# Kernel optimization log

Hardware: AMD Instinct MI355X
Metric: run time of the kernel (lower is better)

## Reference

```python
import jax, jax.numpy as jnp
import numpy as np

B, L, D = 16, 1024, 768

def setup_inputs() -> dict:
    key = jax.random.key(0)
    ks = jax.random.split(key, 6)
    s = 1.0 / np.sqrt(D)  # torch Linear default init scale
    return {
        "h": jax.random.normal(ks[0], (B, L, D), dtype=jnp.float32),
        "q": jax.random.normal(ks[1], (B, L, D), dtype=jnp.float32),
        "w1_w": jax.random.uniform(ks[2], (L, D), jnp.float32, -s, s),
        "w1_b": jax.random.uniform(ks[3], (L,), jnp.float32, -s, s),
        "w2_w": jax.random.uniform(ks[4], (L, D), jnp.float32, -s, s),
        "w2_b": jax.random.uniform(ks[5], (L,), jnp.float32, -s, s),
    }

def reference(h, q, w1_w, w1_b, w2_w, w2_b):
    # w1h: [B, L, l], w2q: [B, L, l] -> permuted [B, l, L]
    w1h = jnp.einsum('bsd,ld->bsl', h, w1_w) + w1_b
    w2q = jnp.einsum('btd,ld->btl', q, w2_w) + w2_b
    w3hq = jnp.einsum('bsd,btd->bst', h, q)           # [B, L, L]
    a = w1h + jnp.swapaxes(w2q, 1, 2) + w3hq          # [B, L, L]
    p = jax.nn.softmax(a, axis=2)
    c = jnp.einsum('bst,btd->bsd', p, q)              # [B, L, D]
    m = jnp.max(a, axis=2)                            # [B, L]
    p2 = jax.nn.softmax(m, axis=1)                    # [B, L]
    qc = h * p2[:, :, None]                           # [B, L, D]
    return jnp.concatenate([h, c, h * c, qc * c], axis=2)  # [B, L, 4D]
```

## Files before the change

### kernel.cpp

```cpp
#include <hip/hip_runtime.h>
#include <stdint.h>

#define B_  16
#define L_  1024
#define D_  768
#define K1_ 1536

typedef unsigned short u16;
typedef __attribute__((ext_vector_type(4))) float f32x4;
typedef __attribute__((ext_vector_type(8))) _Float16 f16x8;

__device__ __forceinline__ u16 f2h(float x){
    return __builtin_bit_cast(u16, (_Float16)x);
}

__device__ __forceinline__ void gload_lds16(const void* g, void* l){
    __builtin_amdgcn_global_load_lds((const __attribute__((address_space(1))) void*)g,
                                     (__attribute__((address_space(3))) void*)l, 16, 0, 0);
}

__global__ __launch_bounds__(256) void prep(const float* __restrict__ h, const float* __restrict__ q,
    const float* __restrict__ w1w, const float* __restrict__ w2w,
    u16* __restrict__ hH, u16* __restrict__ wH, u16* __restrict__ qH,
    u16* __restrict__ w1h, u16* __restrict__ qT, int b0, int nb)
{
    __shared__ float tile[32][33];
    int bb = blockIdx.z, bg = b0 + bb;
    int t0 = blockIdx.x * 32, d0 = blockIdx.y * 32;
    int tid = threadIdx.x;
    int r  = tid >> 3;
    int c4 = (tid & 7) * 4;
    int t = t0 + r, d = d0 + c4;
    size_t goff = (size_t)t * D_ + d;

    float4 qv  = *(const float4*)(q   + (size_t)bg * L_ * D_ + goff);
    float4 hv  = *(const float4*)(h   + (size_t)bg * L_ * D_ + goff);
    float4 w2v = *(const float4*)(w2w + goff);

    tile[r][c4 + 0] = qv.x; tile[r][c4 + 1] = qv.y;
    tile[r][c4 + 2] = qv.z; tile[r][c4 + 3] = qv.w;

    size_t o = ((size_t)bb * L_ + t) * D_ + d;
    ushort4 a;
    a.x = f2h(hv.x); a.y = f2h(hv.y); a.z = f2h(hv.z); a.w = f2h(hv.w);
    *(ushort4*)(hH + o) = a;
    a.x = f2h(hv.x + w2v.x); a.y = f2h(hv.y + w2v.y);
    a.z = f2h(hv.z + w2v.z); a.w = f2h(hv.w + w2v.w);
    *(ushort4*)(wH + o) = a;
    a.x = f2h(qv.x); a.y = f2h(qv.y); a.z = f2h(qv.z); a.w = f2h(qv.w);
    *(ushort4*)(qH + o) = a;
    if (bb == 0){
        float4 w1v = *(const float4*)(w1w + goff);
        a.x = f2h(w1v.x); a.y = f2h(w1v.y); a.z = f2h(w1v.z); a.w = f2h(w1v.w);
        *(ushort4*)(w1h + goff) = a;
    }
    __syncthreads();
    int dr = tid >> 3;
    int tc = (tid & 7) * 4;
    ushort4 b;
    b.x = f2h(tile[tc + 0][dr]); b.y = f2h(tile[tc + 1][dr]);
    b.z = f2h(tile[tc + 2][dr]); b.w = f2h(tile[tc + 3][dr]);
    *(ushort4*)(qT + (size_t)bb * D_ * L_ + (size_t)(d0 + dr) * L_ + t0 + tc) = b;
}

__global__ __launch_bounds__(256) void gemm1(
    const u16* __restrict__ hH, const u16* __restrict__ wH,
    const u16* __restrict__ qH, const u16* __restrict__ w1h,
    const float* __restrict__ w1b, const float* __restrict__ w2b,
    u16* __restrict__ pT, float* __restrict__ mT, float* __restrict__ sT)
{
    __shared__ u16 ldsA[128 * 64];
    __shared__ u16 ldsB[128 * 64];
    int nwg = gridDim.x;
    int o = blockIdx.x;
    int wg = (o & 7) * (nwg >> 3) + (o >> 3);
    int bb = wg >> 6;
    int tl = wg & 63;
    int sm = tl >> 3, tn = tl & 7;
    int s0 = sm * 128, t0 = tn * 128;
    int tid = threadIdx.x;
    int lane = tid & 63, wid = tid >> 6;
    int wm = wid >> 1, wn = wid & 1;
    int l15 = lane & 15, l4 = lane >> 4;

    const u16* hHb = hH + (size_t)bb * L_ * D_;
    const u16* wHb = wH + (size_t)bb * L_ * D_;
    const u16* qHb = qH + (size_t)bb * L_ * D_;

    f32x4 acc[4][4];
    #pragma unroll
    for (int m = 0; m < 4; m++)
        #pragma unroll
        for (int n = 0; n < 4; n++)
            acc[m][n] = (f32x4){0.f, 0.f, 0.f, 0.f};

    for (int kb = 0; kb < K1_; kb += 64){
        bool inH = (kb < D_);
        const u16* Asrc = inH ? hHb : wHb;
        const u16* Bsrc = inH ? w1h : qHb;
        int koff = inH ? kb : (kb - D_);
        #pragma unroll
        for (int j = 0; j < 4; j++){
            int n = j * 256 + tid;
            int row = n >> 3, c = n & 7;
            int cc = c ^ (row & 7);
            int k = koff + cc * 8;
            gload_lds16(Asrc + (size_t)(s0 + row) * D_ + k, &ldsA[(j * 256 + wid * 64) * 8]);
            gload_lds16(Bsrc + (size_t)(t0 + row) * D_ + k, &ldsB[(j * 256 + wid * 64) * 8]);
        }
        __syncthreads();
        #pragma unroll
        for (int kk = 0; kk < 2; kk++){
            f16x8 af[4], bf[4];
            #pragma unroll
            for (int m = 0; m < 4; m++){
                int row = wm * 64 + m * 16 + l15;
                int c = kk * 4 + l4;
                af[m] = *(const f16x8*)&ldsA[(row * 8 + (c ^ (row & 7))) * 8];
            }
            #pragma unroll
            for (int n = 0; n < 4; n++){
                int row = wn * 64 + n * 16 + l15;
                int c = kk * 4 + l4;
                bf[n] = *(const f16x8*)&ldsB[(row * 8 + (c ^ (row & 7))) * 8];
            }
            #pragma unroll
            for (int m = 0; m < 4; m++)
                #pragma unroll
                for (int n = 0; n < 4; n++)
                    acc[m][n] = __builtin_amdgcn_mfma_f32_16x16x32_f16(af[m], bf[n], acc[m][n], 0, 0, 0);
        }
        __syncthreads();
    }

    u16* pRow = pT + (size_t)bb * L_ * L_;
    #pragma unroll
    for (int m = 0; m < 4; m++){
        #pragma unroll
        for (int r = 0; r < 4; r++){
            int s = s0 + wm * 64 + m * 16 + l4 * 4 + r;
            float w2v = w2b[s];
            float v[4];
            float tmax = -1e30f;
            #pragma unroll
            for (int n = 0; n < 4; n++){
                int tcol = t0 + wn * 64 + n * 16 + l15;
                v[n] = acc[m][n][r] + w1b[tcol] + w2v;
                tmax = fmaxf(tmax, v[n]);
            }
            #pragma unroll
            for (int o2 = 1; o2 < 16; o2 <<= 1)
                tmax = fmaxf(tmax, __shfl_xor(tmax, o2));
            float e[4];
            float gsum = 0.f;
            #pragma unroll
            for (int n = 0; n < 4; n++){
                e[n] = __expf(v[n] - tmax);
                gsum += e[n];
            }
            #pragma unroll
            for (int n = 0; n < 4; n++){
                int tcol = t0 + wn * 64 + n * 16 + l15;
                pRow[(size_t)s * L_ + tcol] = f2h(e[n]);
            }
            #pragma unroll
            for (int o2 = 1; o2 < 16; o2 <<= 1)
                gsum += __shfl_xor(gsum, o2);
            if (l15 == 0){
                size_t mo = ((size_t)bb * L_ + s) * 16 + tn * 2 + wn;
                mT[mo] = tmax;
                sT[mo] = gsum;
            }
        }
    }
}

__global__ __launch_bounds__(1024) void p2k(const float* __restrict__ mT, const float* __restrict__ sT,
                                            float* __restrict__ p2, float* __restrict__ sc, int b0)
{
    __shared__ float red[16];
    int bb = blockIdx.x, bg = b0 + bb;
    int tid = threadIdx.x;
    const float4* mv = (const float4*)(mT + ((size_t)bb * L_ + tid) * 16);
    float4 m0 = mv[0], m1 = mv[1], m2 = mv[2], m3 = mv[3];
    float mj[16] = {m0.x, m0.y, m0.z, m0.w, m1.x, m1.y, m1.z, m1.w,
                    m2.x, m2.y, m2.z, m2.w, m3.x, m3.y, m3.z, m3.w};
    float v = mj[0];
    #pragma unroll
    for (int i = 1; i < 16; i++) v = fmaxf(v, mj[i]);

    float mx = v;
    #pragma unroll
    for (int o = 32; o; o >>= 1) mx = fmaxf(mx, __shfl_xor(mx, o));
    if ((tid & 63) == 0) red[tid >> 6] = mx;
    __syncthreads();
    float m2g = red[0];
    #pragma unroll
    for (int i = 1; i < 16; i++) m2g = fmaxf(m2g, red[i]);
    float e = __expf(v - m2g);
    float sum = e;
    #pragma unroll
    for (int o = 32; o; o >>= 1) sum += __shfl_xor(sum, o);
    __syncthreads();
    if ((tid & 63) == 0) red[tid >> 6] = sum;
    __syncthreads();
    float st = 0.f;
    #pragma unroll
    for (int i = 0; i < 16; i++) st += red[i];
    p2[(size_t)bg * L_ + tid] = e / st;

    const float4* sv = (const float4*)(sT + ((size_t)bb * L_ + tid) * 16);
    float4 s0v = sv[0], s1v = sv[1], s2v = sv[2], s3v = sv[3];
    float sj[16] = {s0v.x, s0v.y, s0v.z, s0v.w, s1v.x, s1v.y, s1v.z, s1v.w,
                    s2v.x, s2v.y, s2v.z, s2v.w, s3v.x, s3v.y, s3v.z, s3v.w};
    float ej[16];
    float S = 0.f;
    #pragma unroll
    for (int j = 0; j < 16; j++){
        ej[j] = __expf(mj[j] - v);
        S += sj[j] * ej[j];
    }
    float invS = 1.0f / S;
    float* scb = sc + (size_t)bb * 16 * L_;
    #pragma unroll
    for (int j = 0; j < 16; j++)
        scb[j * L_ + tid] = ej[j] * invS;
}

__global__ __launch_bounds__(256) void gemm2(const u16* __restrict__ pT, const u16* __restrict__ qT,
    const float* __restrict__ sc, float* __restrict__ out, int b0)
{
    __shared__ u16 ldsA[128 * 64];
    __shared__ u16 ldsB[128 * 64];
    int nwg = gridDim.x;
    int o = blockIdx.x;
    int wg = (o & 7) * (nwg >> 3) + (o >> 3);
    int bb = wg / 48;
    int tl = wg % 48;
    int sm = tl / 6, dn = tl % 6;
    int s0 = sm * 128, d0 = dn * 128;
    int tid = threadIdx.x;
    int lane = tid & 63, wid = tid >> 6;
    int wm = wid >> 1, wn = wid & 1;
    int l15 = lane & 15, l4 = lane >> 4;

    const u16* Ab = pT + (size_t)bb * L_ * L_;
    const u16* Bb = qT + (size_t)bb * D_ * L_;
    const float* scb = sc + (size_t)bb * 16 * L_;

    f32x4 acc[4][4];
    #pragma unroll
    for (int m = 0; m < 4; m++)
        #pragma unroll
        for (int n = 0; n < 4; n++)
            acc[m][n] = (f32x4){0.f, 0.f, 0.f, 0.f};

    for (int kb = 0; kb < L_; kb += 64){
        int jg = kb >> 6;
        #pragma unroll
        for (int j = 0; j < 4; j++){
            int n = j * 256 + tid;
            int row = n >> 3, c = n & 7;
            int cc = c ^ (row & 7);
            gload_lds16(Ab + (size_t)(s0 + row) * L_ + kb + cc * 8, &ldsA[(j * 256 + wid * 64) * 8]);
        }
        #pragma unroll
        for (int j = 0; j < 4; j++){
            int n = j * 256 + tid;
            int row = n >> 3, c = n & 7;
            int cc = c ^ (row & 7);
            gload_lds16(Bb + (size_t)(d0 + row) * L_ + kb + cc * 8, &ldsB[(j * 256 + wid * 64) * 8]);
        }
        _Float16 sch[4];
        #pragma unroll
        for (int m = 0; m < 4; m++)
            sch[m] = (_Float16)scb[(size_t)jg * L_ + s0 + wm * 64 + m * 16 + l15];
        __syncthreads();
        #pragma unroll
        for (int kk = 0; kk < 2; kk++){
            f16x8 af[4], bf[4];
            #pragma unroll
            for (int m = 0; m < 4; m++){
                int row = wm * 64 + m * 16 + l15;
                int c = kk * 4 + l4;
                af[m] = *(const f16x8*)&ldsA[(row * 8 + (c ^ (row & 7))) * 8];
                af[m] = af[m] * sch[m];
            }
            #pragma unroll
            for (int n = 0; n < 4; n++){
                int row = wn * 64 + n * 16 + l15;
                int c = kk * 4 + l4;
                bf[n] = *(const f16x8*)&ldsB[(row * 8 + (c ^ (row & 7))) * 8];
            }
            #pragma unroll
            for (int m = 0; m < 4; m++)
                #pragma unroll
                for (int n = 0; n < 4; n++)
                    acc[m][n] = __builtin_amdgcn_mfma_f32_16x16x32_f16(af[m], bf[n], acc[m][n], 0, 0, 0);
        }
        __syncthreads();
    }

    float* oC = out + ((size_t)(b0 + bb) * L_) * (4 * D_) + D_;
    #pragma unroll
    for (int m = 0; m < 4; m++){
        int sbase = s0 + wm * 64 + m * 16 + l4 * 4;
        #pragma unroll
        for (int r = 0; r < 4; r++){
            int s = sbase + r;
            #pragma unroll
            for (int n = 0; n < 4; n++){
                int d = d0 + wn * 64 + n * 16 + l15;
                oC[(size_t)s * (4 * D_) + d] = acc[m][n][r];
            }
        }
    }
}

__global__ __launch_bounds__(192) void epi(const float* __restrict__ h,
    const float* __restrict__ p2, float* __restrict__ out, int b0)
{
    int rowid = blockIdx.x;
    int bb = rowid >> 10, s = rowid & 1023;
    int bg = b0 + bb;
    float p2v = p2[(size_t)bg * L_ + s];
    const float* hR = h + ((size_t)bg * L_ + s) * D_;
    float* oR = out + ((size_t)bg * L_ + s) * (4 * D_);
    int d = threadIdx.x * 4;
    float4 cv = *(const float4*)(oR + D_ + d);
    float4 hv = *(const float4*)(hR + d);
    float4 hc = {hv.x * cv.x, hv.y * cv.y, hv.z * cv.z, hv.w * cv.w};
    float4 qc = {p2v * hc.x, p2v * hc.y, p2v * hc.z, p2v * hc.w};
    *(float4*)(oR + d)          = hv;
    *(float4*)(oR + 2 * D_ + d) = hc;
    *(float4*)(oR + 3 * D_ + d) = qc;
}

extern "C" void kernel_launch(void* const* d_in, const int* in_sizes, int n_in,
                              void* d_out, int out_size, void* d_ws, size_t ws_size,
                              hipStream_t stream)
{
    const float* h   = (const float*)d_in[0];
    const float* q   = (const float*)d_in[1];
    const float* w1w = (const float*)d_in[2];
    const float* w1b = (const float*)d_in[3];
    const float* w2w = (const float*)d_in[4];
    const float* w2b = (const float*)d_in[5];
    float* out = (float*)d_out;

    const size_t szPlane = (size_t)L_ * D_ * 2;
    const size_t szM     = (size_t)B_ * L_ * 4;
    const size_t perB_pT = (size_t)L_ * L_ * 2;
    const size_t perB_s  = (size_t)L_ * 16 * 4;
    const size_t perB = 4 * szPlane + perB_pT + 3 * perB_s;
    const size_t fixed = szPlane + szM;

    int NB = 1;
    if (ws_size > fixed){
        size_t nbc = (ws_size - fixed) / perB;
        NB = (nbc >= 16) ? 16 : (nbc < 1 ? 1 : (int)nbc);
    }

    char* p = (char*)d_ws;
    u16*   w1h  = (u16*)p;   p += szPlane;
    float* p2   = (float*)p; p += szM;
    float* mT   = (float*)p; p += perB_s * NB;
    float* sT   = (float*)p; p += perB_s * NB;
    float* sc   = (float*)p; p += perB_s * NB;
    u16*   hH   = (u16*)p;   p += szPlane * NB;
    u16*   wH   = (u16*)p;   p += szPlane * NB;
    u16*   qH   = (u16*)p;   p += szPlane * NB;
    u16*   qT   = (u16*)p;   p += szPlane * NB;
    u16*   pT   = (u16*)p;

    for (int b0 = 0; b0 < B_; b0 += NB){
        int nb = (B_ - b0 < NB) ? (B_ - b0) : NB;
        prep  <<<dim3(32, 24, nb), 256, 0, stream>>>(h, q, w1w, w2w, hH, wH, qH, w1h, qT, b0, nb);
        gemm1 <<<dim3(64 * nb), 256, 0, stream>>>(hH, wH, qH, w1h, w1b, w2b, pT, mT, sT);
        p2k   <<<dim3(nb), 1024, 0, stream>>>(mT, sT, p2, sc, b0);
        gemm2 <<<dim3(48 * nb), 256, 0, stream>>>(pT, qT, sc, out, b0);
        epi   <<<dim3(nb * 1024), 192, 0, stream>>>(h, p2, out, b0);
    }
}
```

Before: 217.6 us.

## Enlarge gemm1 tiles to 256x256 with double-buffered LDS prefetch

```diff
diff --git a/kernel.cpp b/kernel.cpp
--- a/kernel.cpp
+++ b/kernel.cpp
@@ -63,88 +63,106 @@
     *(ushort4*)(qT + (size_t)bb * D_ * L_ + (size_t)(d0 + dr) * L_ + t0 + tc) = b;
 }
 
-__global__ __launch_bounds__(256) void gemm1(
+__global__ __launch_bounds__(512) void gemm1(
     const u16* __restrict__ hH, const u16* __restrict__ wH,
     const u16* __restrict__ qH, const u16* __restrict__ w1h,
     const float* __restrict__ w1b, const float* __restrict__ w2b,
     u16* __restrict__ pT, float* __restrict__ mT, float* __restrict__ sT)
 {
-    __shared__ u16 ldsA[128 * 64];
-    __shared__ u16 ldsB[128 * 64];
+    __shared__ u16 ldsA[2][256 * 64];
+    __shared__ u16 ldsB[2][256 * 64];
     int nwg = gridDim.x;
     int o = blockIdx.x;
     int wg = (o & 7) * (nwg >> 3) + (o >> 3);
-    int bb = wg >> 6;
-    int tl = wg & 63;
-    int sm = tl >> 3, tn = tl & 7;
-    int s0 = sm * 128, t0 = tn * 128;
+    int bb = wg >> 4;
+    int tl = wg & 15;
+    int smb = tl >> 2, tnb = tl & 3;
+    int s0 = smb * 256, t0 = tnb * 256;
     int tid = threadIdx.x;
     int lane = tid & 63, wid = tid >> 6;
-    int wm = wid >> 1, wn = wid & 1;
+    int wm2 = wid >> 2, wn2 = wid & 3;
     int l15 = lane & 15, l4 = lane >> 4;
 
     const u16* hHb = hH + (size_t)bb * L_ * D_;
     const u16* wHb = wH + (size_t)bb * L_ * D_;
     const u16* qHb = qH + (size_t)bb * L_ * D_;
 
-    f32x4 acc[4][4];
-    #pragma unroll
-    for (int m = 0; m < 4; m++)
+    f32x4 acc[8][4];
+    #pragma unroll
+    for (int m = 0; m < 8; m++)
         #pragma unroll
         for (int n = 0; n < 4; n++)
             acc[m][n] = (f32x4){0.f, 0.f, 0.f, 0.f};
 
-    for (int kb = 0; kb < K1_; kb += 64){
+    auto stage = [&](int t){
+        int kb = t * 64;
         bool inH = (kb < D_);
-        const u16* Asrc = inH ? hHb : wHb;
-        const u16* Bsrc = inH ? w1h : qHb;
+        const u16* As = inH ? hHb : wHb;
+        const u16* Bs = inH ? w1h : qHb;
         int koff = inH ? kb : (kb - D_);
-        #pragma unroll
-        for (int j = 0; j < 4; j++){
-            int n = j * 256 + tid;
-            int row = n >> 3, c = n & 7;
+        int buf = t & 1;
+        #pragma unroll
+        for (int q = 0; q < 4; q++){
+            int idx = q * 512 + tid;
+            int row = idx >> 3, c = idx & 7;
             int cc = c ^ (row & 7);
-            int k = koff + cc * 8;
-            gload_lds16(Asrc + (size_t)(s0 + row) * D_ + k, &ldsA[(j * 256 + wid * 64) * 8]);
-            gload_lds16(Bsrc + (size_t)(t0 + row) * D_ + k, &ldsB[(j * 256 + wid * 64) * 8]);
-        }
-        __syncthreads();
+            int dst = (q * 512 + wid * 64) * 8;
+            gload_lds16(As + (size_t)(s0 + row) * D_ + koff + cc * 8, &ldsA[buf][dst]);
+            gload_lds16(Bs + (size_t)(t0 + row) * D_ + koff + cc * 8, &ldsB[buf][dst]);
+        }
+    };
+
+    stage(0);
+    asm volatile("s_waitcnt vmcnt(0)" ::: "memory");
+    __builtin_amdgcn_s_barrier();
+
+    for (int t = 0; t < 24; t++){
+        if (t + 1 < 24) stage(t + 1);
+        int bsel = t & 1;
         #pragma unroll
         for (int kk = 0; kk < 2; kk++){
-            f16x8 af[4], bf[4];
-            #pragma unroll
-            for (int m = 0; m < 4; m++){
-                int row = wm * 64 + m * 16 + l15;
+            f16x8 bf[4];
+            #pragma unroll
+            for (int n = 0; n < 4; n++){
+                int row = wn2 * 64 + n * 16 + l15;
                 int c = kk * 4 + l4;
-                af[m] = *(const f16x8*)&ldsA[(row * 8 + (c ^ (row & 7))) * 8];
-            }
-            #pragma unroll
-            for (int n = 0; n < 4; n++){
-                int row = wn * 64 + n * 16 + l15;
-                int c = kk * 4 + l4;
-                bf[n] = *(const f16x8*)&ldsB[(row * 8 + (c ^ (row & 7))) * 8];
-            }
-            #pragma unroll
-            for (int m = 0; m < 4; m++)
+                bf[n] = *(const f16x8*)&ldsB[bsel][(row * 8 + (c ^ (row & 7))) * 8];
+            }
+            #pragma unroll
+            for (int mh = 0; mh < 2; mh++){
+                f16x8 af[4];
                 #pragma unroll
-                for (int n = 0; n < 4; n++)
-                    acc[m][n] = __builtin_amdgcn_mfma_f32_16x16x32_f16(af[m], bf[n], acc[m][n], 0, 0, 0);
-        }
-        __syncthreads();
+                for (int mi = 0; mi < 4; mi++){
+                    int row = wm2 * 128 + (mh * 4 + mi) * 16 + l15;
+                    int c = kk * 4 + l4;
+                    af[mi] = *(const f16x8*)&ldsA[bsel][(row * 8 + (c ^ (row & 7))) * 8];
+                }
+                __builtin_amdgcn_s_setprio(1);
+                #pragma unroll
+                for (int mi = 0; mi < 4; mi++)
+                    #pragma unroll
+                    for (int n = 0; n < 4; n++)
+                        acc[mh * 4 + mi][n] = __builtin_amdgcn_mfma_f32_16x16x32_f16(
+                            af[mi], bf[n], acc[mh * 4 + mi][n], 0, 0, 0);
+                __builtin_amdgcn_s_setprio(0);
+            }
+        }
+        asm volatile("s_waitcnt vmcnt(0)" ::: "memory");
+        __builtin_amdgcn_s_barrier();
     }
 
     u16* pRow = pT + (size_t)bb * L_ * L_;
     #pragma unroll
-    for (int m = 0; m < 4; m++){
+    for (int m = 0; m < 8; m++){
         #pragma unroll
         for (int r = 0; r < 4; r++){
-            int s = s0 + wm * 64 + m * 16 + l4 * 4 + r;
+            int s = s0 + wm2 * 128 + m * 16 + l4 * 4 + r;
             float w2v = w2b[s];
             float v[4];
             float tmax = -1e30f;
             #pragma unroll
             for (int n = 0; n < 4; n++){
-                int tcol = t0 + wn * 64 + n * 16 + l15;
+                int tcol = t0 + wn2 * 64 + n * 16 + l15;
                 v[n] = acc[m][n][r] + w1b[tcol] + w2v;
                 tmax = fmaxf(tmax, v[n]);
             }
@@ -160,14 +178,14 @@
             }
             #pragma unroll
             for (int n = 0; n < 4; n++){
-                int tcol = t0 + wn * 64 + n * 16 + l15;
+                int tcol = t0 + wn2 * 64 + n * 16 + l15;
                 pRow[(size_t)s * L_ + tcol] = f2h(e[n]);
             }
             #pragma unroll
             for (int o2 = 1; o2 < 16; o2 <<= 1)
                 gsum += __shfl_xor(gsum, o2);
             if (l15 == 0){
-                size_t mo = ((size_t)bb * L_ + s) * 16 + tn * 2 + wn;
+                size_t mo = ((size_t)bb * L_ + s) * 16 + tnb * 4 + wn2;
                 mT[mo] = tmax;
                 sT[mo] = gsum;
             }
@@ -376,7 +394,7 @@
     for (int b0 = 0; b0 < B_; b0 += NB){
         int nb = (B_ - b0 < NB) ? (B_ - b0) : NB;
         prep  <<<dim3(32, 24, nb), 256, 0, stream>>>(h, q, w1w, w2w, hH, wH, qH, w1h, qT, b0, nb);
-        gemm1 <<<dim3(64 * nb), 256, 0, stream>>>(hH, wH, qH, w1h, w1b, w2b, pT, mT, sT);
+        gemm1 <<<dim3(16 * nb), 512, 0, stream>>>(hH, wH, qH, w1h, w1b, w2b, pT, mT, sT);
         p2k   <<<dim3(nb), 1024, 0, stream>>>(mT, sT, p2, sc, b0);
         gemm2 <<<dim3(48 * nb), 256, 0, stream>>>(pT, qT, sc, out, b0);
         epi   <<<dim3(nb * 1024), 192, 0, stream>>>(h, p2, out, b0);
```

After: 205.6 us. -5.5%, faster.
